# Performance work log

Measured on AMD Instinct MI355X. Metric: run time of the kernel, lower is better.

The kernel has to match this reference:

```python
import math
import jax, jax.numpy as jnp
import numpy as np

H = 16  # n_heads


def setup_inputs() -> dict:
    key = jax.random.key(0)
    ks = jax.random.split(key, 12)
    b, n, dm = 4, 1024, 1024
    s = 1.0 / math.sqrt(dm)
    inp = {
        'query': jax.random.normal(ks[0], (b, n, dm), jnp.float32),
        'key':   jax.random.normal(ks[1], (b, n, dm), jnp.float32),
        'value': jax.random.normal(ks[2], (b, n, dm), jnp.float32),
        'Wq': jax.random.normal(ks[3], (dm, dm), jnp.float32) * s,
        'bq': jnp.zeros((dm,), jnp.float32),
        'Wk': jax.random.normal(ks[4], (dm, dm), jnp.float32) * s,
        'bk': jnp.zeros((dm,), jnp.float32),
        'Wv': jax.random.normal(ks[5], (dm, dm), jnp.float32) * s,
        'bv': jnp.zeros((dm,), jnp.float32),
        'Wo': jax.random.normal(ks[6], (dm, dm), jnp.float32) * s,
        'bo': jnp.zeros((dm,), jnp.float32),
    }
    return inp


def reference(query, key, value, Wq, bq, Wk, bk, Wv, bv, Wo, bo):
    b, n, dm = query.shape
    dk = dm // H

    def proj(x, W, bias):
        # Linear(d_model,d_model) then split heads: [b,n,dm] -> [b,h,n,dk]
        y = x @ W.T + bias
        return y.reshape(b, n, H, dk).transpose(0, 2, 1, 3)

    q = proj(query, Wq, bq)
    k = proj(key, Wk, bk)
    v = proj(value, Wv, bv)

    scores = jnp.einsum('bhid,bhjd->bhij', q, k) / math.sqrt(dk)  # [b,h,n,n]
    p_attn = jax.nn.softmax(scores, axis=-1)
    # softmax(ones) along last dim is exactly uniform 1/n
    p_ident = jnp.full_like(scores, 1.0 / n)
    rnd = jax.random.normal(jax.random.key(42), scores.shape, scores.dtype)
    p_rand = jax.nn.softmax(rnd, axis=-1)

    # FAITHFUL to source: einsum('b h i j, b h i d -> b h i d', p, value)
    # i.e. value scaled by row-sum of the attention probs (== value up to numerics)
    def weight(p):
        return v * jnp.sum(p, axis=-1, keepdims=True)  # [b,h,n,dk]

    x = weight(p_attn)
    y = weight(p_ident)
    z = weight(p_rand)

    def merge(t):  # [b,h,n,dk] -> [b,n,dm]
        return t.transpose(0, 2, 1, 3).reshape(b, n, dm)

    return (merge(x) @ Wo.T + bo, merge(y), merge(z))
```

## Files before the change

### kernel.cpp

```cpp
#include <hip/hip_runtime.h>
#include <hip/hip_bf16.h>
#include <stdint.h>

using bf16 = __hip_bfloat16;
typedef __attribute__((ext_vector_type(8))) __bf16 bf16x8;
typedef __attribute__((ext_vector_type(4))) float f32x4;

static __device__ __forceinline__ bf16 f2b(float x) { return __float2bfloat16(x); }
static __device__ __forceinline__ uint32_t pack2(float a, float b) {
    bf16 ha = f2b(a), hb = f2b(b);
    return (uint32_t)(*(const uint16_t*)&ha) | ((uint32_t)(*(const uint16_t*)&hb) << 16);
}

__global__ __launch_bounds__(256) void prep_w_kernel(
    const float* __restrict__ Wv, const float* __restrict__ Wo,
    bf16* __restrict__ Wv_b, bf16* __restrict__ Wo_b, bf16* __restrict__ WvT_b,
    int nbWo, int dm)
{
    __shared__ bf16 tile[32][34];
    const int b = blockIdx.x;
    const int tid = threadIdx.x;

    if (b < nbWo) {
        const size_t i = ((size_t)b * 256 + tid) * 8;
        const float4 v0 = *(const float4*)(Wo + i);
        const float4 v1 = *(const float4*)(Wo + i + 4);
        uint4 u = { pack2(v0.x, v0.y), pack2(v0.z, v0.w),
                    pack2(v1.x, v1.y), pack2(v1.z, v1.w) };
        *(uint4*)(Wo_b + i) = u;
    } else {
        const int t = b - nbWo;
        const int tpr = dm / 32;
        const int i0 = (t / tpr) * 32, j0 = (t % tpr) * 32;
        const int tx = tid & 31, ty = tid >> 5;
        #pragma unroll
        for (int p = 0; p < 4; ++p) {
            const int r = ty + p * 8;
            const bf16 h = f2b(Wv[(size_t)(i0 + r) * dm + j0 + tx]);
            Wv_b[(size_t)(i0 + r) * dm + j0 + tx] = h;
            tile[r][tx] = h;
        }
        __syncthreads();
        #pragma unroll
        for (int p = 0; p < 4; ++p) {
            const int c = ty + p * 8;
            WvT_b[(size_t)(j0 + c) * dm + i0 + tx] = tile[tx][c];
        }
    }
}

__global__ __launch_bounds__(256, 4) void mix_kernel(
    const bf16* __restrict__ A, const bf16* __restrict__ B,
    const float* __restrict__ value, const float* __restrict__ Wo,
    const float* __restrict__ bv, const float* __restrict__ bo,
    bf16* __restrict__ Wc_b, bf16* __restrict__ value_b, float* __restrict__ bc,
    int nbWc, int nbVal, int dm)
{
    __shared__ bf16 As[64 * 64];
    __shared__ bf16 Bs[64 * 64];

    const int blk = blockIdx.x;
    const int tid = threadIdx.x;

    if (blk < nbWc) {
        const int K = dm, N = dm;
        const int tpr = dm / 64;
        const int bm = (blk / tpr) * 64, bn = (blk % tpr) * 64;
        const int lane = tid & 63;
        const int wave = tid >> 6;
        const int wm = (wave >> 1) * 32;
        const int wn = (wave & 1) * 32;

        f32x4 acc[2][2] = {};

        const int s0 = wave * 128 + lane;
        const int s1 = s0 + 64;
        const int r0 = s0 >> 3, r1 = s1 >> 3;
        const int p0 = (s0 & 7) ^ (r0 & 7);
        const int p1 = (s1 & 7) ^ (r1 & 7);
        const bf16* gA0 = A + (size_t)(bm + r0) * K + p0 * 8;
        const bf16* gA1 = A + (size_t)(bm + r1) * K + p1 * 8;
        const bf16* gB0 = B + (size_t)(bn + r0) * K + p0 * 8;
        const bf16* gB1 = B + (size_t)(bn + r1) * K + p1 * 8;
        bf16* lA0 = As + s0 * 8;
        bf16* lA1 = As + s1 * 8;
        bf16* lB0 = Bs + s0 * 8;
        bf16* lB1 = Bs + s1 * 8;

        const int fr = lane & 15;
        const int fkc = lane >> 4;

        for (int k0 = 0; k0 < K; k0 += 64) {
            __builtin_amdgcn_global_load_lds(
                (const __attribute__((address_space(1))) void*)(gA0 + k0),
                (__attribute__((address_space(3))) void*)lA0, 16, 0, 0);
            __builtin_amdgcn_global_load_lds(
                (const __attribute__((address_space(1))) void*)(gA1 + k0),
                (__attribute__((address_space(3))) void*)lA1, 16, 0, 0);
            __builtin_amdgcn_global_load_lds(
                (const __attribute__((address_space(1))) void*)(gB0 + k0),
                (__attribute__((address_space(3))) void*)lB0, 16, 0, 0);
            __builtin_amdgcn_global_load_lds(
                (const __attribute__((address_space(1))) void*)(gB1 + k0),
                (__attribute__((address_space(3))) void*)lB1, 16, 0, 0);
            __syncthreads();

            #pragma unroll
            for (int kk = 0; kk < 2; ++kk) {
                const int xsw = ((kk * 4 + fkc) ^ (fr & 7)) * 8;
                bf16x8 af[2], bg[2];
                #pragma unroll
                for (int u = 0; u < 2; ++u) {
                    af[u] = *(const bf16x8*)(As + (wm + u * 16 + fr) * 64 + xsw);
                    bg[u] = *(const bf16x8*)(Bs + (wn + u * 16 + fr) * 64 + xsw);
                }
                #pragma unroll
                for (int i = 0; i < 2; ++i)
                    #pragma unroll
                    for (int j = 0; j < 2; ++j)
                        acc[i][j] = __builtin_amdgcn_mfma_f32_16x16x32_bf16(
                            af[i], bg[j], acc[i][j], 0, 0, 0);
            }
            __syncthreads();
        }

        const int quad = lane >> 4;
        #pragma unroll
        for (int j = 0; j < 2; ++j) {
            const int col = bn + wn + j * 16 + fr;
            #pragma unroll
            for (int i = 0; i < 2; ++i) {
                const int row0 = bm + wm + i * 16 + quad * 4;
                #pragma unroll
                for (int r = 0; r < 4; ++r)
                    Wc_b[(size_t)(row0 + r) * N + col] = f2b(acc[i][j][r]);
            }
        }
    } else if (blk < nbWc + nbVal) {
        const size_t i = ((size_t)(blk - nbWc) * 256 + tid) * 8;
        const float4 v0 = *(const float4*)(value + i);
        const float4 v1 = *(const float4*)(value + i + 4);
        uint4 u = { pack2(v0.x, v0.y), pack2(v0.z, v0.w),
                    pack2(v1.x, v1.y), pack2(v1.z, v1.w) };
        *(uint4*)(value_b + i) = u;
    } else {
        const int lane = tid & 63;
        const int wave = tid >> 6;
        const int row = (blk - nbWc - nbVal) * 4 + wave;
        const float* wrow = Wo + (size_t)row * dm;
        float s = 0.f;
        for (int k = lane * 4; k < dm; k += 256) {
            const float4 w = *(const float4*)(wrow + k);
            const float4 x = *(const float4*)(bv + k);
            s += w.x * x.x + w.y * x.y + w.z * x.z + w.w * x.w;
        }
        #pragma unroll
        for (int off = 32; off >= 1; off >>= 1) s += __shfl_down(s, off, 64);
        if (lane == 0) bc[row] = s + bo[row];
    }
}

#define TM 128
#define TN 128
#define BK 32

__global__ __launch_bounds__(256, 4) void gemm_fused(
    const bf16* __restrict__ A, const bf16* __restrict__ Bcat,
    const float* __restrict__ bv, const float* __restrict__ bc,
    float* __restrict__ out0, float* __restrict__ out1, float* __restrict__ out2,
    int M, int dm)
{
    __shared__ bf16 As[TM * BK];
    __shared__ bf16 Bs[TN * BK];
    __shared__ float Es[4][16 * 68];

    const int K = dm;
    const int tid = threadIdx.x;
    const int lane = tid & 63;
    const int wave = tid >> 6;
    const int wm = (wave >> 1) * 64;
    const int wn = (wave & 1) * 64;
    const int bm = blockIdx.x * TM;
    const int bn = blockIdx.y * TN;

    f32x4 acc[4][4] = {};

    const int s0 = wave * 128 + lane;
    const int s1 = s0 + 64;
    const int r0 = s0 >> 2, r1 = s1 >> 2;
    const int p0 = (s0 & 3) ^ (r0 & 3) ^ ((r0 >> 2) & 3);
    const int p1 = (s1 & 3) ^ (r1 & 3) ^ ((r1 >> 2) & 3);
    const bf16* gA0 = A + (size_t)(bm + r0) * K + p0 * 8;
    const bf16* gA1 = A + (size_t)(bm + r1) * K + p1 * 8;
    const bf16* gB0 = Bcat + (size_t)(bn + r0) * K + p0 * 8;
    const bf16* gB1 = Bcat + (size_t)(bn + r1) * K + p1 * 8;
    bf16* lA0 = As + s0 * 8;
    bf16* lA1 = As + s1 * 8;
    bf16* lB0 = Bs + s0 * 8;
    bf16* lB1 = Bs + s1 * 8;

    const int fr = lane & 15;
    const int fkc = lane >> 4;
    const int xsw = fkc ^ (fr & 3) ^ ((fr >> 2) & 3);

    for (int k0 = 0; k0 < K; k0 += BK) {
        __builtin_amdgcn_global_load_lds(
            (const __attribute__((address_space(1))) void*)(gA0 + k0),
            (__attribute__((address_space(3))) void*)lA0, 16, 0, 0);
        __builtin_amdgcn_global_load_lds(
            (const __attribute__((address_space(1))) void*)(gA1 + k0),
            (__attribute__((address_space(3))) void*)lA1, 16, 0, 0);
        __builtin_amdgcn_global_load_lds(
            (const __attribute__((address_space(1))) void*)(gB0 + k0),
            (__attribute__((address_space(3))) void*)lB0, 16, 0, 0);
        __builtin_amdgcn_global_load_lds(
            (const __attribute__((address_space(1))) void*)(gB1 + k0),
            (__attribute__((address_space(3))) void*)lB1, 16, 0, 0);
        __syncthreads();

        bf16x8 af[4], bg[4];
        #pragma unroll
        for (int t = 0; t < 4; ++t) {
            af[t] = *(const bf16x8*)(As + (wm + t * 16 + fr) * BK + xsw * 8);
            bg[t] = *(const bf16x8*)(Bs + (wn + t * 16 + fr) * BK + xsw * 8);
        }
        #pragma unroll
        for (int i = 0; i < 4; ++i)
            #pragma unroll
            for (int j = 0; j < 4; ++j)
                acc[i][j] = __builtin_amdgcn_mfma_f32_16x16x32_bf16(
                    af[i], bg[j], acc[i][j], 0, 0, 0);
        __syncthreads();
    }

    const bool second = (bn >= dm);
    const int colbase = bn + wn - (second ? dm : 0);
    const float* bias = second ? bc : bv;
    float* o0 = second ? out0 : out1;
    float* o1 = second ? nullptr : out2;

    float bb[4];
    #pragma unroll
    for (int j = 0; j < 4; ++j) bb[j] = bias[colbase + j * 16 + fr];

    float* E = &Es[wave][0];
    const int quad = lane >> 4;
    const int cc = (lane & 15) * 4;

    #pragma unroll
    for (int i = 0; i < 4; ++i) {
        #pragma unroll
        for (int j = 0; j < 4; ++j)
            #pragma unroll
            for (int r = 0; r < 4; ++r)
                E[(quad * 4 + r) * 68 + j * 16 + fr] = acc[i][j][r] + bb[j];
        #pragma unroll
        for (int ph = 0; ph < 4; ++ph) {
            const int row = quad * 4 + ph;
            const float4 v = *(const float4*)(E + row * 68 + cc);
            const size_t gi = (size_t)(bm + wm + i * 16 + row) * dm + colbase + cc;
            *(float4*)(o0 + gi) = v;
            if (o1) *(float4*)(o1 + gi) = v;
        }
    }
}

__global__ __launch_bounds__(256) void gemm_f32_naive(
    const float* __restrict__ A, const float* __restrict__ B,
    const float* __restrict__ bias,
    float* __restrict__ C0, float* __restrict__ C1,
    int M, int N, int K)
{
    const size_t idx = (size_t)blockIdx.x * 256 + threadIdx.x;
    if (idx >= (size_t)M * N) return;
    const int row = (int)(idx / N), col = (int)(idx % N);
    const float* a = A + (size_t)row * K;
    const float* b = B + (size_t)col * K;
    float s = bias ? bias[col] : 0.0f;
    for (int k = 0; k < K; ++k) s += a[k] * b[k];
    C0[idx] = s;
    if (C1) C1[idx] = s;
}

extern "C" void kernel_launch(void* const* d_in, const int* in_sizes, int n_in,
                              void* d_out, int out_size, void* d_ws, size_t ws_size,
                              hipStream_t stream)
{
    const float* value = (const float*)d_in[2];
    const float* Wv    = (const float*)d_in[7];
    const float* bv    = (const float*)d_in[8];
    const float* Wo    = (const float*)d_in[9];
    const float* bo    = (const float*)d_in[10];

    const int dm = in_sizes[8];
    const int M  = in_sizes[2] / dm;
    const size_t MN = (size_t)M * dm;

    float* out0 = (float*)d_out;
    float* out1 = out0 + MN;
    float* out2 = out1 + MN;

    const size_t dm2 = (size_t)dm * dm;
    const size_t need = MN * 2 + dm2 * 2 * 4 + (size_t)dm * 4;
    const bool ok = (ws_size >= need) && (M % TM == 0) && (dm % TM == 0) &&
                    (MN % 2048 == 0) && (dm2 % 2048 == 0) &&
                    (dm % 64 == 0) && (dm % 4 == 0);
    if (ok) {
        char* ws = (char*)d_ws;
        bf16* value_b = (bf16*)ws;   ws += MN * 2;
        bf16* Wv_b    = (bf16*)ws;   ws += dm2 * 2;
        bf16* Wc_b    = (bf16*)ws;   ws += dm2 * 2;
        bf16* Wo_b    = (bf16*)ws;   ws += dm2 * 2;
        bf16* WvT_b   = (bf16*)ws;   ws += dm2 * 2;
        float* bc     = (float*)ws;

        const int nbWo  = (int)(dm2 / 2048);
        const int nbT   = (dm / 32) * (dm / 32);
        prep_w_kernel<<<nbWo + nbT, 256, 0, stream>>>(
            Wv, Wo, Wv_b, Wo_b, WvT_b, nbWo, dm);

        const int nbWc  = (dm / 64) * (dm / 64);
        const int nbVal = (int)(MN / 2048);
        const int nbBc  = dm / 4;
        mix_kernel<<<nbWc + nbVal + nbBc, 256, 0, stream>>>(
            Wo_b, WvT_b, value, Wo, bv, bo, Wc_b, value_b, bc,
            nbWc, nbVal, dm);

        dim3 grid(M / TM, 2 * dm / TN);
        gemm_fused<<<grid, 256, 0, stream>>>(value_b, Wv_b, bv, bc,
                                             out0, out1, out2, M, dm);
    } else {
        const int nblk = (int)((MN + 255) / 256);
        gemm_f32_naive<<<nblk, 256, 0, stream>>>(value, Wv, bv, out1, out2, M, dm, dm);
        gemm_f32_naive<<<nblk, 256, 0, stream>>>(out1, Wo, bo, out0, nullptr, M, dm, dm);
    }
}
```

Baseline: 154.2 us.

## Fuse Wo bf16 conversion into mix GEMM and deepen main GEMM K-tile

The separate pass that converted Wo to bf16 is removed. The Wc GEMM in mix_kernel now loads Wo as fp32, packs it to bf16 in registers and writes it into swizzled LDS, which cuts one full-matrix write and read and one workspace buffer. The main fused GEMM raises BK from 32 to 64 with an 8-way XOR swizzle, so it does half as many barriers per K. In exchange its occupancy hint drops to 2 blocks per CU and it uses more LDS per block.

```diff
diff --git a/kernel.cpp b/kernel.cpp
--- a/kernel.cpp
+++ b/kernel.cpp
@@ -13,44 +13,32 @@
 }
 
 __global__ __launch_bounds__(256) void prep_w_kernel(
-    const float* __restrict__ Wv, const float* __restrict__ Wo,
-    bf16* __restrict__ Wv_b, bf16* __restrict__ Wo_b, bf16* __restrict__ WvT_b,
-    int nbWo, int dm)
+    const float* __restrict__ Wv,
+    bf16* __restrict__ Wv_b, bf16* __restrict__ WvT_b, int dm)
 {
     __shared__ bf16 tile[32][34];
-    const int b = blockIdx.x;
+    const int t = blockIdx.x;
     const int tid = threadIdx.x;
-
-    if (b < nbWo) {
-        const size_t i = ((size_t)b * 256 + tid) * 8;
-        const float4 v0 = *(const float4*)(Wo + i);
-        const float4 v1 = *(const float4*)(Wo + i + 4);
-        uint4 u = { pack2(v0.x, v0.y), pack2(v0.z, v0.w),
-                    pack2(v1.x, v1.y), pack2(v1.z, v1.w) };
-        *(uint4*)(Wo_b + i) = u;
-    } else {
-        const int t = b - nbWo;
-        const int tpr = dm / 32;
-        const int i0 = (t / tpr) * 32, j0 = (t % tpr) * 32;
-        const int tx = tid & 31, ty = tid >> 5;
-        #pragma unroll
-        for (int p = 0; p < 4; ++p) {
-            const int r = ty + p * 8;
-            const bf16 h = f2b(Wv[(size_t)(i0 + r) * dm + j0 + tx]);
-            Wv_b[(size_t)(i0 + r) * dm + j0 + tx] = h;
-            tile[r][tx] = h;
-        }
-        __syncthreads();
-        #pragma unroll
-        for (int p = 0; p < 4; ++p) {
-            const int c = ty + p * 8;
-            WvT_b[(size_t)(j0 + c) * dm + i0 + tx] = tile[tx][c];
-        }
+    const int tpr = dm / 32;
+    const int i0 = (t / tpr) * 32, j0 = (t % tpr) * 32;
+    const int tx = tid & 31, ty = tid >> 5;
+    #pragma unroll
+    for (int p = 0; p < 4; ++p) {
+        const int r = ty + p * 8;
+        const bf16 h = f2b(Wv[(size_t)(i0 + r) * dm + j0 + tx]);
+        Wv_b[(size_t)(i0 + r) * dm + j0 + tx] = h;
+        tile[r][tx] = h;
+    }
+    __syncthreads();
+    #pragma unroll
+    for (int p = 0; p < 4; ++p) {
+        const int c = ty + p * 8;
+        WvT_b[(size_t)(j0 + c) * dm + i0 + tx] = tile[tx][c];
     }
 }
 
 __global__ __launch_bounds__(256, 4) void mix_kernel(
-    const bf16* __restrict__ A, const bf16* __restrict__ B,
+    const bf16* __restrict__ B,
     const float* __restrict__ value, const float* __restrict__ Wo,
     const float* __restrict__ bv, const float* __restrict__ bo,
     bf16* __restrict__ Wc_b, bf16* __restrict__ value_b, float* __restrict__ bc,
@@ -78,36 +66,43 @@
         const int r0 = s0 >> 3, r1 = s1 >> 3;
         const int p0 = (s0 & 7) ^ (r0 & 7);
         const int p1 = (s1 & 7) ^ (r1 & 7);
-        const bf16* gA0 = A + (size_t)(bm + r0) * K + p0 * 8;
-        const bf16* gA1 = A + (size_t)(bm + r1) * K + p1 * 8;
         const bf16* gB0 = B + (size_t)(bn + r0) * K + p0 * 8;
         const bf16* gB1 = B + (size_t)(bn + r1) * K + p1 * 8;
-        bf16* lA0 = As + s0 * 8;
-        bf16* lA1 = As + s1 * 8;
         bf16* lB0 = Bs + s0 * 8;
         bf16* lB1 = Bs + s1 * 8;
 
+        const int sa0 = tid, sa1 = tid + 256;
+        const int ra0 = sa0 >> 3, pa0 = (sa0 & 7) ^ (ra0 & 7);
+        const int ra1 = sa1 >> 3, pa1 = (sa1 & 7) ^ (ra1 & 7);
+        const float* gA0 = Wo + (size_t)(bm + ra0) * K + pa0 * 8;
+        const float* gA1 = Wo + (size_t)(bm + ra1) * K + pa1 * 8;
+
         const int fr = lane & 15;
         const int fkc = lane >> 4;
+        const int xb = fr & 7;
 
         for (int k0 = 0; k0 < K; k0 += 64) {
-            __builtin_amdgcn_global_load_lds(
-                (const __attribute__((address_space(1))) void*)(gA0 + k0),
-                (__attribute__((address_space(3))) void*)lA0, 16, 0, 0);
-            __builtin_amdgcn_global_load_lds(
-                (const __attribute__((address_space(1))) void*)(gA1 + k0),
-                (__attribute__((address_space(3))) void*)lA1, 16, 0, 0);
             __builtin_amdgcn_global_load_lds(
                 (const __attribute__((address_space(1))) void*)(gB0 + k0),
                 (__attribute__((address_space(3))) void*)lB0, 16, 0, 0);
             __builtin_amdgcn_global_load_lds(
                 (const __attribute__((address_space(1))) void*)(gB1 + k0),
                 (__attribute__((address_space(3))) void*)lB1, 16, 0, 0);
+            const float4 a0 = *(const float4*)(gA0 + k0);
+            const float4 a1 = *(const float4*)(gA0 + k0 + 4);
+            const float4 a2 = *(const float4*)(gA1 + k0);
+            const float4 a3 = *(const float4*)(gA1 + k0 + 4);
+            uint4 u0 = { pack2(a0.x, a0.y), pack2(a0.z, a0.w),
+                         pack2(a1.x, a1.y), pack2(a1.z, a1.w) };
+            uint4 u1 = { pack2(a2.x, a2.y), pack2(a2.z, a2.w),
+                         pack2(a3.x, a3.y), pack2(a3.z, a3.w) };
+            *(uint4*)(As + sa0 * 8) = u0;
+            *(uint4*)(As + sa1 * 8) = u1;
             __syncthreads();
 
             #pragma unroll
             for (int kk = 0; kk < 2; ++kk) {
-                const int xsw = ((kk * 4 + fkc) ^ (fr & 7)) * 8;
+                const int xsw = ((kk * 4 + fkc) ^ xb) * 8;
                 bf16x8 af[2], bg[2];
                 #pragma unroll
                 for (int u = 0; u < 2; ++u) {
@@ -162,9 +157,9 @@
 
 #define TM 128
 #define TN 128
-#define BK 32
-
-__global__ __launch_bounds__(256, 4) void gemm_fused(
+#define BK 64
+
+__global__ __launch_bounds__(256, 2) void gemm_fused(
     const bf16* __restrict__ A, const bf16* __restrict__ Bcat,
     const float* __restrict__ bv, const float* __restrict__ bc,
     float* __restrict__ out0, float* __restrict__ out1, float* __restrict__ out2,
@@ -185,51 +180,52 @@
 
     f32x4 acc[4][4] = {};
 
-    const int s0 = wave * 128 + lane;
-    const int s1 = s0 + 64;
-    const int r0 = s0 >> 2, r1 = s1 >> 2;
-    const int p0 = (s0 & 3) ^ (r0 & 3) ^ ((r0 >> 2) & 3);
-    const int p1 = (s1 & 3) ^ (r1 & 3) ^ ((r1 >> 2) & 3);
-    const bf16* gA0 = A + (size_t)(bm + r0) * K + p0 * 8;
-    const bf16* gA1 = A + (size_t)(bm + r1) * K + p1 * 8;
-    const bf16* gB0 = Bcat + (size_t)(bn + r0) * K + p0 * 8;
-    const bf16* gB1 = Bcat + (size_t)(bn + r1) * K + p1 * 8;
-    bf16* lA0 = As + s0 * 8;
-    bf16* lA1 = As + s1 * 8;
-    bf16* lB0 = Bs + s0 * 8;
-    bf16* lB1 = Bs + s1 * 8;
+    const bf16* gA[4]; const bf16* gB[4];
+    bf16* lA[4]; bf16* lB[4];
+    #pragma unroll
+    for (int q = 0; q < 4; ++q) {
+        const int s = wave * 256 + q * 64 + lane;
+        const int r = s >> 3;
+        const int p = (s & 7) ^ (r & 7);
+        gA[q] = A + (size_t)(bm + r) * K + p * 8;
+        gB[q] = Bcat + (size_t)(bn + r) * K + p * 8;
+        lA[q] = As + s * 8;
+        lB[q] = Bs + s * 8;
+    }
 
     const int fr = lane & 15;
     const int fkc = lane >> 4;
-    const int xsw = fkc ^ (fr & 3) ^ ((fr >> 2) & 3);
+    const int xb = fr & 7;
 
     for (int k0 = 0; k0 < K; k0 += BK) {
-        __builtin_amdgcn_global_load_lds(
-            (const __attribute__((address_space(1))) void*)(gA0 + k0),
-            (__attribute__((address_space(3))) void*)lA0, 16, 0, 0);
-        __builtin_amdgcn_global_load_lds(
-            (const __attribute__((address_space(1))) void*)(gA1 + k0),
-            (__attribute__((address_space(3))) void*)lA1, 16, 0, 0);
-        __builtin_amdgcn_global_load_lds(
-            (const __attribute__((address_space(1))) void*)(gB0 + k0),
-            (__attribute__((address_space(3))) void*)lB0, 16, 0, 0);
-        __builtin_amdgcn_global_load_lds(
-            (const __attribute__((address_space(1))) void*)(gB1 + k0),
-            (__attribute__((address_space(3))) void*)lB1, 16, 0, 0);
+        #pragma unroll
+        for (int q = 0; q < 4; ++q)
+            __builtin_amdgcn_global_load_lds(
+                (const __attribute__((address_space(1))) void*)(gA[q] + k0),
+                (__attribute__((address_space(3))) void*)lA[q], 16, 0, 0);
+        #pragma unroll
+        for (int q = 0; q < 4; ++q)
+            __builtin_amdgcn_global_load_lds(
+                (const __attribute__((address_space(1))) void*)(gB[q] + k0),
+                (__attribute__((address_space(3))) void*)lB[q], 16, 0, 0);
         __syncthreads();
 
-        bf16x8 af[4], bg[4];
-        #pragma unroll
-        for (int t = 0; t < 4; ++t) {
-            af[t] = *(const bf16x8*)(As + (wm + t * 16 + fr) * BK + xsw * 8);
-            bg[t] = *(const bf16x8*)(Bs + (wn + t * 16 + fr) * BK + xsw * 8);
-        }
-        #pragma unroll
-        for (int i = 0; i < 4; ++i)
-            #pragma unroll
-            for (int j = 0; j < 4; ++j)
-                acc[i][j] = __builtin_amdgcn_mfma_f32_16x16x32_bf16(
-                    af[i], bg[j], acc[i][j], 0, 0, 0);
+        #pragma unroll
+        for (int kk = 0; kk < 2; ++kk) {
+            const int xsw = ((kk * 4 + fkc) ^ xb) * 8;
+            bf16x8 af[4], bg[4];
+            #pragma unroll
+            for (int t = 0; t < 4; ++t) {
+                af[t] = *(const bf16x8*)(As + (wm + t * 16 + fr) * BK + xsw);
+                bg[t] = *(const bf16x8*)(Bs + (wn + t * 16 + fr) * BK + xsw);
+            }
+            #pragma unroll
+            for (int i = 0; i < 4; ++i)
+                #pragma unroll
+                for (int j = 0; j < 4; ++j)
+                    acc[i][j] = __builtin_amdgcn_mfma_f32_16x16x32_bf16(
+                        af[i], bg[j], acc[i][j], 0, 0, 0);
+        }
         __syncthreads();
     }
 
@@ -301,7 +297,7 @@
     float* out2 = out1 + MN;
 
     const size_t dm2 = (size_t)dm * dm;
-    const size_t need = MN * 2 + dm2 * 2 * 4 + (size_t)dm * 4;
+    const size_t need = MN * 2 + dm2 * 2 * 3 + (size_t)dm * 4;
     const bool ok = (ws_size >= need) && (M % TM == 0) && (dm % TM == 0) &&
                     (MN % 2048 == 0) && (dm2 % 2048 == 0) &&
                     (dm % 64 == 0) && (dm % 4 == 0);
@@ -310,20 +306,17 @@
         bf16* value_b = (bf16*)ws;   ws += MN * 2;
         bf16* Wv_b    = (bf16*)ws;   ws += dm2 * 2;
         bf16* Wc_b    = (bf16*)ws;   ws += dm2 * 2;
-        bf16* Wo_b    = (bf16*)ws;   ws += dm2 * 2;
         bf16* WvT_b   = (bf16*)ws;   ws += dm2 * 2;
         float* bc     = (float*)ws;
 
-        const int nbWo  = (int)(dm2 / 2048);
-        const int nbT   = (dm / 32) * (dm / 32);
-        prep_w_kernel<<<nbWo + nbT, 256, 0, stream>>>(
-            Wv, Wo, Wv_b, Wo_b, WvT_b, nbWo, dm);
+        const int nbT = (dm / 32) * (dm / 32);
+        prep_w_kernel<<<nbT, 256, 0, stream>>>(Wv, Wv_b, WvT_b, dm);
 
         const int nbWc  = (dm / 64) * (dm / 64);
         const int nbVal = (int)(MN / 2048);
         const int nbBc  = dm / 4;
         mix_kernel<<<nbWc + nbVal + nbBc, 256, 0, stream>>>(
-            Wo_b, WvT_b, value, Wo, bv, bo, Wc_b, value_b, bc,
+            WvT_b, value, Wo, bv, bo, Wc_b, value_b, bc,
             nbWc, nbVal, dm);
 
         dim3 grid(M / TM, 2 * dm / TN);
```

Result: faster. 150.6 us (-2.3%).
